# Kernel tuning notes

Hardware: AMD Instinct MI355X
Metric: run time of the kernel (lower is better)

Reference implementation:

```python
import jax, jax.numpy as jnp
import numpy as np

B, T, C, H = 8, 2048, 1024, 64  # batch, seq (== block_size), n_embd, head_size


def setup_inputs() -> dict:
    key = jax.random.key(0)
    k1, k2, k3, k4 = jax.random.split(key, 4)
    x = jax.random.normal(k1, (B, T, C), dtype=jnp.float32)
    scale = 0.02
    Wk = jax.random.normal(k2, (H, C), dtype=jnp.float32) * scale  # nn.Linear weight [out,in]
    Wq = jax.random.normal(k3, (H, C), dtype=jnp.float32) * scale
    Wv = jax.random.normal(k4, (H, C), dtype=jnp.float32) * scale
    return {"x": x, "Wk": Wk, "Wq": Wq, "Wv": Wv}


def reference(x, Wk, Wq, Wv):
    # k, q, v projections (bias-free linears): x @ W.T
    k = jnp.einsum('btc,hc->bth', x, Wk)
    q = jnp.einsum('btc,hc->bth', x, Wq)
    v = jnp.einsum('btc,hc->bth', x, Wv)
    # NOTE: source MULTIPLIES by sqrt(head_size) (faithful to original code)
    wei = jnp.einsum('bth,bsh->bts', q, k) * (H ** 0.5)  # [B,T,T]
    causal = jnp.tril(jnp.ones((T, T), dtype=bool))
    wei = jnp.where(causal, wei, -jnp.inf)
    wei = jax.nn.softmax(wei, axis=-1)
    # dropout_value = 0.0 -> identity (deterministic baseline)
    out = jnp.einsum('bts,bsh->bth', wei, v)  # [B,T,H]
    return out
```

## Files before the change

kernel.cpp:

```cpp
#include <hip/hip_runtime.h>

#define BB 8
#define TT 2048
#define CC 1024
#define HH 64
#define MM (BB * TT)

typedef _Float16 half8 __attribute__((ext_vector_type(8)));
typedef _Float16 half4 __attribute__((ext_vector_type(4)));
typedef float floatx4 __attribute__((ext_vector_type(4)));

template <int CTRL>
__device__ __forceinline__ float dpp_max_step(float x)
{
    union { float f; int i; } u, v;
    u.f = x;
    v.i = __builtin_amdgcn_update_dpp(u.i, u.i, CTRL, 0xf, 0xf, false);
    return fmaxf(x, v.f);
}
__device__ __forceinline__ float rowmax16(float x)
{
    x = dpp_max_step<0x128>(x);
    x = dpp_max_step<0x124>(x);
    x = dpp_max_step<0x122>(x);
    x = dpp_max_step<0x121>(x);
    return x;
}

__device__ __forceinline__ void gll16(const float* g, float* l)
{
    __builtin_amdgcn_global_load_lds(
        (const __attribute__((address_space(1))) unsigned int*)g,
        (__attribute__((address_space(3))) unsigned int*)l, 16, 0, 0);
}

#define MEMFENCE asm volatile("" ::: "memory")

__global__ __launch_bounds__(256)
void w_pack(const float* __restrict__ Wk, const float* __restrict__ Wq,
            const float* __restrict__ Wv, _Float16* __restrict__ Wp)
{
    const int idx = (blockIdx.x * 256 + threadIdx.x) * 8;
    const int c   = idx / 6144;
    const int rm  = idx - c * 6144;
    const int row = rm >> 5;
    const int kk  = rm & 31;
    const int which = row >> 6;
    const float* __restrict__ src = (which == 0) ? Wq : ((which == 1) ? Wk : Wv);
    const float scale = (which == 0) ? 8.0f : 1.0f;
    const int srow = row & 63;
    const int k = c * 32 + kk;
    const float4 a = *reinterpret_cast<const float4*>(&src[srow * 1024 + k]);
    const float4 b = *reinterpret_cast<const float4*>(&src[srow * 1024 + k + 4]);
    const half8 o = { (_Float16)(a.x * scale), (_Float16)(a.y * scale),
                      (_Float16)(a.z * scale), (_Float16)(a.w * scale),
                      (_Float16)(b.x * scale), (_Float16)(b.y * scale),
                      (_Float16)(b.z * scale), (_Float16)(b.w * scale) };
    *reinterpret_cast<half8*>(&Wp[idx]) = o;
}

__global__ __launch_bounds__(512, 2)
void qkv9(const float* __restrict__ x, const _Float16* __restrict__ Wp,
          _Float16* __restrict__ q16, _Float16* __restrict__ Kp,
          _Float16* __restrict__ Vp)
{
    __shared__ float xs[4][64][32];

    const int tid  = threadIdx.x;
    const int lane = tid & 63;
    const int w    = tid >> 6;
    const int blk  = blockIdx.x;
    const int m_base = blk * 64;
    const int fm = lane & 15;
    const int fq = lane >> 4;
    const int fk = fq * 8;
    const int fr = fq * 4;
    const int wm = w >> 2;
    const int wn = w & 3;

    const float* gsrc = &x[(size_t)(m_base + w * 8 + (lane >> 3)) * CC
                           + ((lane & 7) ^ (lane >> 3)) * 4];
    float* ldst = &xs[0][w * 8][0];

    const _Float16* wb = &Wp[(wn * 48 + fm) * 32 + fk];

    floatx4 acc[2][3];
    #pragma unroll
    for (int a = 0; a < 2; ++a)
        #pragma unroll
        for (int n = 0; n < 3; ++n)
            #pragma unroll
            for (int r = 0; r < 4; ++r) acc[a][n][r] = 0.0f;

    half8 wA[3], wB[3];

    #pragma unroll
    for (int n = 0; n < 3; ++n)
        wA[n] = *reinterpret_cast<const half8*>(wb + n * 512);
    MEMFENCE;
    gll16(gsrc + 0 * 32, ldst + 0 * 2048);
    gll16(gsrc + 1 * 32, ldst + 1 * 2048);
    gll16(gsrc + 2 * 32, ldst + 2 * 2048);
    asm volatile("s_waitcnt vmcnt(2)" ::: "memory");
    __builtin_amdgcn_s_barrier();
    MEMFENCE;

#define QKV_ITER(c, WUSE, WLOAD, DO_W, DO_X, NWAIT)                            \
    {                                                                          \
        if (DO_W) {                                                            \
            _Pragma("unroll")                                                  \
            for (int n = 0; n < 3; ++n)                                        \
                WLOAD[n] = *reinterpret_cast<const half8*>(                    \
                    wb + (size_t)((c) + 1) * 6144 + n * 512);                  \
        }                                                                      \
        MEMFENCE;                                                              \
        if (DO_X) gll16(gsrc + ((c) + 3) * 32, ldst + (((c) + 3) & 3) * 2048); \
        _Pragma("unroll")                                                      \
        for (int a = 0; a < 2; ++a) {                                          \
            const int rr = wm * 32 + a * 16 + fm;                              \
            const float* rowp = &xs[(c) & 3][rr][0];                           \
            const int sw = fm & 7;                                             \
            const float4 v0 = *reinterpret_cast<const float4*>(                \
                rowp + ((fq * 2 + 0) ^ sw) * 4);                               \
            const float4 v1 = *reinterpret_cast<const float4*>(                \
                rowp + ((fq * 2 + 1) ^ sw) * 4);                               \
            const half8 af = { (_Float16)v0.x, (_Float16)v0.y,                 \
                               (_Float16)v0.z, (_Float16)v0.w,                 \
                               (_Float16)v1.x, (_Float16)v1.y,                 \
                               (_Float16)v1.z, (_Float16)v1.w };               \
            _Pragma("unroll")                                                  \
            for (int n = 0; n < 3; ++n)                                        \
                acc[a][n] = __builtin_amdgcn_mfma_f32_16x16x32_f16(            \
                    af, WUSE[n], acc[a][n], 0, 0, 0);                          \
        }                                                                      \
        asm volatile("s_waitcnt vmcnt(" #NWAIT ")" ::: "memory");              \
        __builtin_amdgcn_s_barrier();                                          \
        MEMFENCE;                                                              \
    }

    for (int cc = 0; cc < 28; cc += 2) {
        QKV_ITER(cc,     wA, wB, true,  true,  8);
        QKV_ITER(cc + 1, wB, wA, true,  true,  8);
    }
    QKV_ITER(28, wA, wB, true,  true,  8);
    QKV_ITER(29, wB, wA, true,  false, 4);
    QKV_ITER(30, wA, wB, true,  false, 0);
    QKV_ITER(31, wB, wA, false, false, 0);
#undef QKV_ITER

    #pragma unroll
    for (int a = 0; a < 2; ++a) {
        const int mt = blk * 4 + wm * 2 + a;
        #pragma unroll
        for (int n = 0; n < 3; ++n) {
            const int col = wn * 48 + n * 16 + fm;
            if (col < 64) {
                #pragma unroll
                for (int r = 0; r < 4; ++r)
                    q16[(size_t)(mt * 16 + fr + r) * HH + col] = (_Float16)acc[a][n][r];
            } else if (col < 128) {
                const int h = col - 64;
                _Float16* kp = &Kp[(size_t)(mt * 2 + (h >> 5)) * 512 + (h & 31)];
                #pragma unroll
                for (int r = 0; r < 4; ++r)
                    kp[(fr + r) * 32] = (_Float16)acc[a][n][r];
            } else {
                const int h = col - 128;
                const half4 pk = { (_Float16)acc[a][n][0], (_Float16)acc[a][n][1],
                                   (_Float16)acc[a][n][2], (_Float16)acc[a][n][3] };
                *reinterpret_cast<half4*>(
                    &Vp[(size_t)((mt >> 2) * 4 + (h >> 4)) * 1024 +
                        ((mt >> 1) & 1) * 512 + fm * 32 + (mt & 1) * 16 + fr]) = pk;
            }
        }
    }
}

__global__ __launch_bounds__(64, 4)
void attn7(const _Float16* __restrict__ q16, const _Float16* __restrict__ Kp,
           const _Float16* __restrict__ Vp, float* __restrict__ out,
           _Float16* __restrict__ Op, float* __restrict__ ml)
{
    __shared__ _Float16 Ps[16 * 68];

    const int bid = blockIdx.x;
    const int it  = 127 - bid / 24;
    const int sub = bid - (127 - it) * 24;
    const int b   = sub & 7;
    const int s   = sub >> 3;

    const int lane = threadIdx.x;
    const int fm = lane & 15;
    const int fq = lane >> 4;
    const int fk = fq * 8;
    const int fr = fq * 4;

    const int Ji = (it >> 2) + 1;
    const int qq = Ji / 3, rem = Ji - qq * 3;
    const int cnt   = qq + (s < rem ? 1 : 0);
    const int start = s * qq + (s < rem ? s : rem);

    const _Float16* __restrict__ kpb = Kp + (size_t)b * TT * HH;
    const _Float16* __restrict__ vpb = Vp + (size_t)b * TT * HH;

    const int qrow = (b * 128 + it) * 16 + fm;
    const half8 qf0 = *reinterpret_cast<const half8*>(&q16[(size_t)qrow * HH + fk]);
    const half8 qf1 = *reinterpret_cast<const half8*>(&q16[(size_t)qrow * HH + 32 + fk]);

    floatx4 O[4], lacc;
    float m_r[4];
    #pragma unroll
    for (int r = 0; r < 4; ++r) {
        m_r[r] = -3.0e38f;
        lacc[r] = 0.0f;
        #pragma unroll
        for (int ht = 0; ht < 4; ++ht) O[ht][r] = 0.0f;
    }
    const half8 ones = { (_Float16)1.f, (_Float16)1.f, (_Float16)1.f, (_Float16)1.f,
                         (_Float16)1.f, (_Float16)1.f, (_Float16)1.f, (_Float16)1.f };

    const int loff = fm * 32 + fk;

    for (int js = 0; js < cnt; ++js) {
        const int jj = start + js;

        floatx4 sa[4];
        #pragma unroll
        for (int nt = 0; nt < 4; ++nt) {
            #pragma unroll
            for (int r = 0; r < 4; ++r) sa[nt][r] = 0.0f;
            const _Float16* kp = &kpb[(size_t)(jj * 4 + nt) * 1024];
            const half8 b0 = *reinterpret_cast<const half8*>(kp + loff);
            const half8 b1 = *reinterpret_cast<const half8*>(kp + 512 + loff);
            sa[nt] = __builtin_amdgcn_mfma_f32_16x16x32_f16(qf0, b0, sa[nt], 0, 0, 0);
            sa[nt] = __builtin_amdgcn_mfma_f32_16x16x32_f16(qf1, b1, sa[nt], 0, 0, 0);
        }

        if (jj == (it >> 2)) {
            const int rbase = it * 16 + fr;
            #pragma unroll
            for (int nt = 0; nt < 4; ++nt) {
                const int col = jj * 64 + nt * 16 + fm;
                #pragma unroll
                for (int r = 0; r < 4; ++r)
                    if (col > rbase + r) sa[nt][r] = -3.0e38f;
            }
        }

        #pragma unroll
        for (int r = 0; r < 4; ++r) {
            float mx = fmaxf(fmaxf(sa[0][r], sa[1][r]), fmaxf(sa[2][r], sa[3][r]));
            mx = rowmax16(mx);
            const float mn = fmaxf(m_r[r], mx);
            const float alpha = __expf(m_r[r] - mn);
            m_r[r] = mn;
            _Float16* pp = &Ps[(fr + r) * 68 + fm];
            pp[0]  = (_Float16)__expf(sa[0][r] - mn);
            pp[16] = (_Float16)__expf(sa[1][r] - mn);
            pp[32] = (_Float16)__expf(sa[2][r] - mn);
            pp[48] = (_Float16)__expf(sa[3][r] - mn);
            lacc[r] *= alpha;
            O[0][r] *= alpha; O[1][r] *= alpha; O[2][r] *= alpha; O[3][r] *= alpha;
        }

        #pragma unroll
        for (int ch = 0; ch < 2; ++ch) {
            const half8 pa = *reinterpret_cast<const half8*>(&Ps[fm * 68 + ch * 32 + fk]);
            lacc = __builtin_amdgcn_mfma_f32_16x16x32_f16(pa, ones, lacc, 0, 0, 0);
            #pragma unroll
            for (int ht = 0; ht < 4; ++ht) {
                const half8 vb = *reinterpret_cast<const half8*>(
                    &vpb[(size_t)(jj * 4 + ht) * 1024 + ch * 512 + loff]);
                O[ht] = __builtin_amdgcn_mfma_f32_16x16x32_f16(pa, vb, O[ht], 0, 0, 0);
            }
        }
    }

    #pragma unroll
    for (int r = 0; r < 4; ++r) {
        const int grow = (b * 128 + it) * 16 + fr + r;
        if (s == 0) {
            #pragma unroll
            for (int ht = 0; ht < 4; ++ht)
                out[(size_t)grow * HH + ht * 16 + fm] = O[ht][r];
        } else {
            #pragma unroll
            for (int ht = 0; ht < 4; ++ht)
                Op[((size_t)(s - 1) * MM + grow) * HH + ht * 16 + fm] = (_Float16)O[ht][r];
        }
        if (fm == 0) {
            ml[((size_t)s * MM + grow) * 2 + 0] = m_r[r];
            ml[((size_t)s * MM + grow) * 2 + 1] = lacc[r];
        }
    }
}

__global__ __launch_bounds__(256)
void combine(float* __restrict__ out, const _Float16* __restrict__ Op,
             const float* __restrict__ ml)
{
    const int tid  = threadIdx.x;
    const int grow = blockIdx.x * 64 + (tid >> 2);
    const int c0   = (tid & 3) * 16;

    const float m0 = ml[(size_t)grow * 2 + 0];
    const float l0 = ml[(size_t)grow * 2 + 1];
    const float m1 = ml[((size_t)MM + grow) * 2 + 0];
    const float l1 = ml[((size_t)MM + grow) * 2 + 1];
    const float m2 = ml[((size_t)2 * MM + grow) * 2 + 0];
    const float l2 = ml[((size_t)2 * MM + grow) * 2 + 1];

    const float M  = fmaxf(m0, fmaxf(m1, m2));
    const float w0 = __expf(m0 - M);
    const float w1 = __expf(m1 - M);
    const float w2 = __expf(m2 - M);
    const float inv = 1.0f / (w0 * l0 + w1 * l1 + w2 * l2);

    #pragma unroll
    for (int i = 0; i < 16; i += 4) {
        float4 o0 = *reinterpret_cast<float4*>(&out[(size_t)grow * HH + c0 + i]);
        const half4 h1 = *reinterpret_cast<const half4*>(&Op[(size_t)grow * HH + c0 + i]);
        const half4 h2 = *reinterpret_cast<const half4*>(&Op[(size_t)MM * HH + (size_t)grow * HH + c0 + i]);
        o0.x = (w0 * o0.x + w1 * (float)h1[0] + w2 * (float)h2[0]) * inv;
        o0.y = (w0 * o0.y + w1 * (float)h1[1] + w2 * (float)h2[1]) * inv;
        o0.z = (w0 * o0.z + w1 * (float)h1[2] + w2 * (float)h2[2]) * inv;
        o0.w = (w0 * o0.w + w1 * (float)h1[3] + w2 * (float)h2[3]) * inv;
        *reinterpret_cast<float4*>(&out[(size_t)grow * HH + c0 + i]) = o0;
    }
}

extern "C" void kernel_launch(void* const* d_in, const int* in_sizes, int n_in,
                              void* d_out, int out_size, void* d_ws, size_t ws_size,
                              hipStream_t stream)
{
    (void)in_sizes; (void)n_in; (void)out_size; (void)ws_size;

    const float* x  = (const float*)d_in[0];
    const float* Wk = (const float*)d_in[1];
    const float* Wq = (const float*)d_in[2];
    const float* Wv = (const float*)d_in[3];
    float* out = (float*)d_out;

    _Float16* base = (_Float16*)d_ws;
    _Float16* q16 = base;
    _Float16* Kp  = base + (size_t)MM * HH;
    _Float16* Vp  = base + (size_t)2 * MM * HH;
    _Float16* Wp  = base + (size_t)3 * MM * HH;
    _Float16* Op  = Wp + 192 * 1024;
    float*    ml  = (float*)(Op + (size_t)2 * MM * HH);

    w_pack<<<dim3(96), dim3(256), 0, stream>>>(Wk, Wq, Wv, Wp);
    qkv9<<<dim3(256), dim3(512), 0, stream>>>(x, Wp, q16, Kp, Vp);
    attn7<<<dim3(3072), dim3(64), 0, stream>>>(q16, Kp, Vp, out, Op, ml);
    combine<<<dim3(256), dim3(256), 0, stream>>>(out, Op, ml);
}
```

Measured before the change: 151.0 us.

## Split QKV projection output columns across blocks with wave-private LDS rows

The QKV projection kernel is replaced. Before, 256 blocks of 512 threads each computed all 192 output columns. Now 1024 blocks of 256 threads each compute one 48-column group, and each wave owns 16 rows of x that only it loads and reads. Because LDS rows are private to a wave, the per-chunk block barrier goes away and the wait for async loads moves ahead of the MFMA. In exchange, every x row is fetched by four different blocks, which relies on L2 or MALL hits to avoid four times the HBM traffic on the fp32 input.

```diff
diff --git a/kernel.cpp b/kernel.cpp
--- a/kernel.cpp
+++ b/kernel.cpp
@@ -59,38 +59,38 @@
     *reinterpret_cast<half8*>(&Wp[idx]) = o;
 }
 
-__global__ __launch_bounds__(512, 2)
-void qkv9(const float* __restrict__ x, const _Float16* __restrict__ Wp,
-          _Float16* __restrict__ q16, _Float16* __restrict__ Kp,
-          _Float16* __restrict__ Vp)
+__global__ __launch_bounds__(256, 4)
+void qkv11(const float* __restrict__ x, const _Float16* __restrict__ Wp,
+           _Float16* __restrict__ q16, _Float16* __restrict__ Kp,
+           _Float16* __restrict__ Vp)
 {
     __shared__ float xs[4][64][32];
 
     const int tid  = threadIdx.x;
     const int lane = tid & 63;
     const int w    = tid >> 6;
-    const int blk  = blockIdx.x;
-    const int m_base = blk * 64;
+    const int bid  = blockIdx.x;
+    const int ms   = bid & 255;
+    const int ng   = bid >> 8;
+    const int m_base = ms * 64;
     const int fm = lane & 15;
     const int fq = lane >> 4;
     const int fk = fq * 8;
     const int fr = fq * 4;
-    const int wm = w >> 2;
-    const int wn = w & 3;
-
-    const float* gsrc = &x[(size_t)(m_base + w * 8 + (lane >> 3)) * CC
-                           + ((lane & 7) ^ (lane >> 3)) * 4];
-    float* ldst = &xs[0][w * 8][0];
-
-    const _Float16* wb = &Wp[(wn * 48 + fm) * 32 + fk];
-
-    floatx4 acc[2][3];
-    #pragma unroll
-    for (int a = 0; a < 2; ++a)
-        #pragma unroll
-        for (int n = 0; n < 3; ++n)
-            #pragma unroll
-            for (int r = 0; r < 4; ++r) acc[a][n][r] = 0.0f;
+
+    const float* gsrc0 = &x[(size_t)(m_base + w * 16 + (lane >> 3)) * CC
+                            + ((lane & 7) ^ (lane >> 3)) * 4];
+    const float* gsrc1 = gsrc0 + 8 * CC;
+    float* ldst0 = &xs[0][w * 16][0];
+    float* ldst1 = &xs[0][w * 16 + 8][0];
+
+    const _Float16* wb = &Wp[(ng * 48 + fm) * 32 + fk];
+
+    floatx4 acc[3];
+    #pragma unroll
+    for (int n = 0; n < 3; ++n)
+        #pragma unroll
+        for (int r = 0; r < 4; ++r) acc[n][r] = 0.0f;
 
     half8 wA[3], wB[3];
 
@@ -98,11 +98,12 @@
     for (int n = 0; n < 3; ++n)
         wA[n] = *reinterpret_cast<const half8*>(wb + n * 512);
     MEMFENCE;
-    gll16(gsrc + 0 * 32, ldst + 0 * 2048);
-    gll16(gsrc + 1 * 32, ldst + 1 * 2048);
-    gll16(gsrc + 2 * 32, ldst + 2 * 2048);
-    asm volatile("s_waitcnt vmcnt(2)" ::: "memory");
-    __builtin_amdgcn_s_barrier();
+    gll16(gsrc0 + 0 * 32, ldst0 + 0 * 2048);
+    gll16(gsrc1 + 0 * 32, ldst1 + 0 * 2048);
+    gll16(gsrc0 + 1 * 32, ldst0 + 1 * 2048);
+    gll16(gsrc1 + 1 * 32, ldst1 + 1 * 2048);
+    gll16(gsrc0 + 2 * 32, ldst0 + 2 * 2048);
+    gll16(gsrc1 + 2 * 32, ldst1 + 2 * 2048);
     MEMFENCE;
 
 #define QKV_ITER(c, WUSE, WLOAD, DO_W, DO_X, NWAIT)                            \
@@ -114,11 +115,14 @@
                     wb + (size_t)((c) + 1) * 6144 + n * 512);                  \
         }                                                                      \
         MEMFENCE;                                                              \
-        if (DO_X) gll16(gsrc + ((c) + 3) * 32, ldst + (((c) + 3) & 3) * 2048); \
-        _Pragma("unroll")                                                      \
-        for (int a = 0; a < 2; ++a) {                                          \
-            const int rr = wm * 32 + a * 16 + fm;                              \
-            const float* rowp = &xs[(c) & 3][rr][0];                           \
+        if (DO_X) {                                                            \
+            const int sl = ((c) + 3) & 3;                                      \
+            gll16(gsrc0 + (size_t)((c) + 3) * 32, ldst0 + sl * 2048);          \
+            gll16(gsrc1 + (size_t)((c) + 3) * 32, ldst1 + sl * 2048);          \
+        }                                                                      \
+        asm volatile("s_waitcnt vmcnt(" #NWAIT ")" ::: "memory");              \
+        {                                                                      \
+            const float* rowp = &xs[(c) & 3][w * 16 + fm][0];                  \
             const int sw = fm & 7;                                             \
             const float4 v0 = *reinterpret_cast<const float4*>(                \
                 rowp + ((fq * 2 + 0) ^ sw) * 4);                               \
@@ -130,44 +134,43 @@
                                (_Float16)v1.z, (_Float16)v1.w };               \
             _Pragma("unroll")                                                  \
             for (int n = 0; n < 3; ++n)                                        \
-                acc[a][n] = __builtin_amdgcn_mfma_f32_16x16x32_f16(            \
-                    af, WUSE[n], acc[a][n], 0, 0, 0);                          \
+                acc[n] = __builtin_amdgcn_mfma_f32_16x16x32_f16(               \
+                    af, WUSE[n], acc[n], 0, 0, 0);                             \
         }                                                                      \
-        asm volatile("s_waitcnt vmcnt(" #NWAIT ")" ::: "memory");              \
-        __builtin_amdgcn_s_barrier();                                          \
         MEMFENCE;                                                              \
     }
 
-    for (int cc = 0; cc < 28; cc += 2) {
-        QKV_ITER(cc,     wA, wB, true,  true,  8);
-        QKV_ITER(cc + 1, wB, wA, true,  true,  8);
-    }
-    QKV_ITER(28, wA, wB, true,  true,  8);
-    QKV_ITER(29, wB, wA, true,  false, 4);
-    QKV_ITER(30, wA, wB, true,  false, 0);
+    QKV_ITER(0, wA, wB, true, true, 9);
+    for (int cc = 1; cc < 27; cc += 2) {
+        QKV_ITER(cc,     wB, wA, true, true, 7);
+        QKV_ITER(cc + 1, wA, wB, true, true, 7);
+    }
+    QKV_ITER(27, wB, wA, true,  true,  7);
+    QKV_ITER(28, wA, wB, true,  true,  7);
+    QKV_ITER(29, wB, wA, true,  false, 5);
+    QKV_ITER(30, wA, wB, true,  false, 3);
     QKV_ITER(31, wB, wA, false, false, 0);
 #undef QKV_ITER
 
-    #pragma unroll
-    for (int a = 0; a < 2; ++a) {
-        const int mt = blk * 4 + wm * 2 + a;
+    {
+        const int mt = ms * 4 + w;
         #pragma unroll
         for (int n = 0; n < 3; ++n) {
-            const int col = wn * 48 + n * 16 + fm;
+            const int col = ng * 48 + n * 16 + fm;
             if (col < 64) {
                 #pragma unroll
                 for (int r = 0; r < 4; ++r)
-                    q16[(size_t)(mt * 16 + fr + r) * HH + col] = (_Float16)acc[a][n][r];
+                    q16[(size_t)(mt * 16 + fr + r) * HH + col] = (_Float16)acc[n][r];
             } else if (col < 128) {
                 const int h = col - 64;
                 _Float16* kp = &Kp[(size_t)(mt * 2 + (h >> 5)) * 512 + (h & 31)];
                 #pragma unroll
                 for (int r = 0; r < 4; ++r)
-                    kp[(fr + r) * 32] = (_Float16)acc[a][n][r];
+                    kp[(fr + r) * 32] = (_Float16)acc[n][r];
             } else {
                 const int h = col - 128;
-                const half4 pk = { (_Float16)acc[a][n][0], (_Float16)acc[a][n][1],
-                                   (_Float16)acc[a][n][2], (_Float16)acc[a][n][3] };
+                const half4 pk = { (_Float16)acc[n][0], (_Float16)acc[n][1],
+                                   (_Float16)acc[n][2], (_Float16)acc[n][3] };
                 *reinterpret_cast<half4*>(
                     &Vp[(size_t)((mt >> 2) * 4 + (h >> 4)) * 1024 +
                         ((mt >> 1) & 1) * 512 + fm * 32 + (mt & 1) * 16 + fr]) = pk;
@@ -350,7 +353,7 @@
     float*    ml  = (float*)(Op + (size_t)2 * MM * HH);
 
     w_pack<<<dim3(96), dim3(256), 0, stream>>>(Wk, Wq, Wv, Wp);
-    qkv9<<<dim3(256), dim3(512), 0, stream>>>(x, Wp, q16, Kp, Vp);
+    qkv11<<<dim3(1024), dim3(256), 0, stream>>>(x, Wp, q16, Kp, Vp);
     attn7<<<dim3(3072), dim3(64), 0, stream>>>(q16, Kp, Vp, out, Op, ml);
     combine<<<dim3(256), dim3(256), 0, stream>>>(out, Op, ml);
 }
```

Result: slower. 156.8 us (+3.8%).

## Stage packed weights through LDS with triple-buffered async loads and skewed K order

Applied to the files above, without the earlier changes.

Weights are now repacked into MFMA fragment order and staged into shared memory with global_load_lds alongside the x tiles, replacing per-wave register double-buffered global loads. The buffering drops from four x slots to three combined x+W slots. Each block starts its K loop at a block-dependent offset so different blocks read different weight chunks at the same time. Larger LDS use lowers occupancy to one block per CU in the launch bounds, which trades latency hiding for fewer redundant global weight reads.

```diff
diff --git a/kernel.cpp b/kernel.cpp
--- a/kernel.cpp
+++ b/kernel.cpp
@@ -33,6 +33,12 @@
         (const __attribute__((address_space(1))) unsigned int*)g,
         (__attribute__((address_space(3))) unsigned int*)l, 16, 0, 0);
 }
+__device__ __forceinline__ void gll16h(const _Float16* g, _Float16* l)
+{
+    __builtin_amdgcn_global_load_lds(
+        (const __attribute__((address_space(1))) unsigned int*)g,
+        (__attribute__((address_space(3))) unsigned int*)l, 16, 0, 0);
+}
 
 #define MEMFENCE asm volatile("" ::: "memory")
 
@@ -40,36 +46,39 @@
 void w_pack(const float* __restrict__ Wk, const float* __restrict__ Wq,
             const float* __restrict__ Wv, _Float16* __restrict__ Wp)
 {
-    const int idx = (blockIdx.x * 256 + threadIdx.x) * 8;
-    const int c   = idx / 6144;
-    const int rm  = idx - c * 6144;
-    const int row = rm >> 5;
-    const int kk  = rm & 31;
-    const int which = row >> 6;
+    const int T   = blockIdx.x * 256 + threadIdx.x;
+    const int c   = T / 768;
+    const int rem = T - c * 768;
+    const int nf  = rem >> 6;
+    const int l   = rem & 63;
+    const int col = nf * 16 + (l & 15);
+    const int k   = c * 32 + (l >> 4) * 8;
+    const int which = col >> 6;
     const float* __restrict__ src = (which == 0) ? Wq : ((which == 1) ? Wk : Wv);
     const float scale = (which == 0) ? 8.0f : 1.0f;
-    const int srow = row & 63;
-    const int k = c * 32 + kk;
+    const int srow = col & 63;
     const float4 a = *reinterpret_cast<const float4*>(&src[srow * 1024 + k]);
     const float4 b = *reinterpret_cast<const float4*>(&src[srow * 1024 + k + 4]);
     const half8 o = { (_Float16)(a.x * scale), (_Float16)(a.y * scale),
                       (_Float16)(a.z * scale), (_Float16)(a.w * scale),
                       (_Float16)(b.x * scale), (_Float16)(b.y * scale),
                       (_Float16)(b.z * scale), (_Float16)(b.w * scale) };
-    *reinterpret_cast<half8*>(&Wp[idx]) = o;
-}
-
-__global__ __launch_bounds__(512, 2)
-void qkv9(const float* __restrict__ x, const _Float16* __restrict__ Wp,
-          _Float16* __restrict__ q16, _Float16* __restrict__ Kp,
-          _Float16* __restrict__ Vp)
-{
-    __shared__ float xs[4][64][32];
+    *reinterpret_cast<half8*>(&Wp[(size_t)T * 8]) = o;
+}
+
+__global__ __launch_bounds__(512, 1)
+void qkv12(const float* __restrict__ x, const _Float16* __restrict__ Wp,
+           _Float16* __restrict__ q16, _Float16* __restrict__ Kp,
+           _Float16* __restrict__ Vp)
+{
+    __shared__ float    xs[3][64][32];
+    __shared__ _Float16 Ws[3][6144];
 
     const int tid  = threadIdx.x;
     const int lane = tid & 63;
     const int w    = tid >> 6;
     const int blk  = blockIdx.x;
+    const int skew = blk & 31;
     const int m_base = blk * 64;
     const int fm = lane & 15;
     const int fq = lane >> 4;
@@ -80,9 +89,9 @@
 
     const float* gsrc = &x[(size_t)(m_base + w * 8 + (lane >> 3)) * CC
                            + ((lane & 7) ^ (lane >> 3)) * 4];
-    float* ldst = &xs[0][w * 8][0];
-
-    const _Float16* wb = &Wp[(wn * 48 + fm) * 32 + fk];
+    float* xbase = &xs[0][w * 8][0];
+
+    const _Float16* wsrc = Wp + lane * 8;
 
     floatx4 acc[2][3];
     #pragma unroll
@@ -92,33 +101,27 @@
             #pragma unroll
             for (int r = 0; r < 4; ++r) acc[a][n][r] = 0.0f;
 
-    half8 wA[3], wB[3];
-
-    #pragma unroll
-    for (int n = 0; n < 3; ++n)
-        wA[n] = *reinterpret_cast<const half8*>(wb + n * 512);
-    MEMFENCE;
-    gll16(gsrc + 0 * 32, ldst + 0 * 2048);
-    gll16(gsrc + 1 * 32, ldst + 1 * 2048);
-    gll16(gsrc + 2 * 32, ldst + 2 * 2048);
-    asm volatile("s_waitcnt vmcnt(2)" ::: "memory");
-    __builtin_amdgcn_s_barrier();
-    MEMFENCE;
-
-#define QKV_ITER(c, WUSE, WLOAD, DO_W, DO_X, NWAIT)                            \
-    {                                                                          \
-        if (DO_W) {                                                            \
-            _Pragma("unroll")                                                  \
-            for (int n = 0; n < 3; ++n)                                        \
-                WLOAD[n] = *reinterpret_cast<const half8*>(                    \
-                    wb + (size_t)((c) + 1) * 6144 + n * 512);                  \
+#define STAGE_X(p, slot) gll16(gsrc + (size_t)(p) * 32, xbase + (slot) * 2048)
+#define STAGE_W(p, slot) do {                                                  \
+        const _Float16* wsp = wsrc + (size_t)(p) * 6144;                       \
+        if (w < 4) {                                                           \
+            gll16h(wsp + (2 * w) * 512,     &Ws[slot][(2 * w) * 512]);         \
+            gll16h(wsp + (2 * w + 1) * 512, &Ws[slot][(2 * w + 1) * 512]);     \
+        } else {                                                               \
+            gll16h(wsp + (4 + w) * 512,     &Ws[slot][(4 + w) * 512]);         \
         }                                                                      \
-        MEMFENCE;                                                              \
-        if (DO_X) gll16(gsrc + ((c) + 3) * 32, ldst + (((c) + 3) & 3) * 2048); \
+    } while (0)
+
+#define COMPUTE(sc) do {                                                       \
+        const half8 wf0 = *reinterpret_cast<const half8*>(                     \
+            &Ws[sc][(wn * 3 + 0) * 512 + lane * 8]);                           \
+        const half8 wf1 = *reinterpret_cast<const half8*>(                     \
+            &Ws[sc][(wn * 3 + 1) * 512 + lane * 8]);                           \
+        const half8 wf2 = *reinterpret_cast<const half8*>(                     \
+            &Ws[sc][(wn * 3 + 2) * 512 + lane * 8]);                           \
         _Pragma("unroll")                                                      \
         for (int a = 0; a < 2; ++a) {                                          \
-            const int rr = wm * 32 + a * 16 + fm;                              \
-            const float* rowp = &xs[(c) & 3][rr][0];                           \
+            const float* rowp = &xs[sc][wm * 32 + a * 16 + fm][0];             \
             const int sw = fm & 7;                                             \
             const float4 v0 = *reinterpret_cast<const float4*>(                \
                 rowp + ((fq * 2 + 0) ^ sw) * 4);                               \
@@ -128,25 +131,41 @@
                                (_Float16)v0.z, (_Float16)v0.w,                 \
                                (_Float16)v1.x, (_Float16)v1.y,                 \
                                (_Float16)v1.z, (_Float16)v1.w };               \
-            _Pragma("unroll")                                                  \
-            for (int n = 0; n < 3; ++n)                                        \
-                acc[a][n] = __builtin_amdgcn_mfma_f32_16x16x32_f16(            \
-                    af, WUSE[n], acc[a][n], 0, 0, 0);                          \
+            acc[a][0] = __builtin_amdgcn_mfma_f32_16x16x32_f16(af, wf0, acc[a][0], 0, 0, 0); \
+            acc[a][1] = __builtin_amdgcn_mfma_f32_16x16x32_f16(af, wf1, acc[a][1], 0, 0, 0); \
+            acc[a][2] = __builtin_amdgcn_mfma_f32_16x16x32_f16(af, wf2, acc[a][2], 0, 0, 0); \
         }                                                                      \
-        asm volatile("s_waitcnt vmcnt(" #NWAIT ")" ::: "memory");              \
+    } while (0)
+
+#define WAITB(NLO, NHI) do {                                                   \
+        if (w < 4) asm volatile("s_waitcnt vmcnt(" #NLO ")" ::: "memory");     \
+        else       asm volatile("s_waitcnt vmcnt(" #NHI ")" ::: "memory");     \
         __builtin_amdgcn_s_barrier();                                          \
         MEMFENCE;                                                              \
-    }
-
-    for (int cc = 0; cc < 28; cc += 2) {
-        QKV_ITER(cc,     wA, wB, true,  true,  8);
-        QKV_ITER(cc + 1, wB, wA, true,  true,  8);
-    }
-    QKV_ITER(28, wA, wB, true,  true,  8);
-    QKV_ITER(29, wB, wA, true,  false, 4);
-    QKV_ITER(30, wA, wB, true,  false, 0);
-    QKV_ITER(31, wB, wA, false, false, 0);
-#undef QKV_ITER
+    } while (0)
+
+    MEMFENCE;
+    STAGE_W(skew, 0);               STAGE_X(skew, 0);
+    STAGE_W((skew + 1) & 31, 1);    STAGE_X((skew + 1) & 31, 1);
+    WAITB(3, 2);
+
+    for (int c = 0; c < 30; ++c) {
+        const int pp = (c + 2 + skew) & 31;
+        const int sl = (c + 2) % 3;
+        STAGE_W(pp, sl);
+        STAGE_X(pp, sl);
+        MEMFENCE;
+        COMPUTE(c % 3);
+        WAITB(3, 2);
+    }
+    COMPUTE(0);
+    WAITB(0, 0);
+    COMPUTE(1);
+
+#undef STAGE_X
+#undef STAGE_W
+#undef COMPUTE
+#undef WAITB
 
     #pragma unroll
     for (int a = 0; a < 2; ++a) {
@@ -350,7 +369,7 @@
     float*    ml  = (float*)(Op + (size_t)2 * MM * HH);
 
     w_pack<<<dim3(96), dim3(256), 0, stream>>>(Wk, Wq, Wv, Wp);
-    qkv9<<<dim3(256), dim3(512), 0, stream>>>(x, Wp, q16, Kp, Vp);
+    qkv12<<<dim3(256), dim3(512), 0, stream>>>(x, Wp, q16, Kp, Vp);
     attn7<<<dim3(3072), dim3(64), 0, stream>>>(q16, Kp, Vp, out, Op, ml);
     combine<<<dim3(256), dim3(256), 0, stream>>>(out, Op, ml);
 }
```

New measurement: 150.9 us. Within noise of the previous version (-0.1%).
